# Kernel optimization log

Measured on AMD Instinct MI355X. Metric: run time of the kernel, lower is better.

## Reference

```python
import jax, jax.numpy as jnp
import numpy as np

N_NODES = 100000
N_EDGES = 1600000
IN_DIM = 48
HID = 16
N_CLASSES = 8


def _sage_conv(x, src, dst, W_l, W_r, b, n_nodes):
    # PyG SAGEConv (aggr='mean', root_weight=True):
    #   out_i = W_l @ mean_{j in N(i)} x_j + b + W_r @ x_i
    msg = x[src]                                              # [E, F]
    agg = jax.ops.segment_sum(msg, dst, num_segments=n_nodes)  # [N, F]
    deg = jax.ops.segment_sum(jnp.ones((src.shape[0],), x.dtype), dst,
                              num_segments=n_nodes)            # [N]
    agg = agg / jnp.maximum(deg, 1.0)[:, None]
    return agg @ W_l.T + b + x @ W_r.T


def setup_inputs() -> dict:
    key = jax.random.key(0)
    ks = jax.random.split(key, 10)
    def lin(k, out_d, in_d):
        s = 1.0 / np.sqrt(in_d)
        return jax.random.uniform(k, (out_d, in_d), jnp.float32, -s, s)
    x = jax.random.normal(ks[0], (N_NODES, IN_DIM), jnp.float32)
    edge_index = jax.random.randint(ks[1], (2, N_EDGES), 0, N_NODES, jnp.int64)
    return {
        "x": x,
        "edge_index": edge_index,
        "W1_l": lin(ks[2], HID, IN_DIM), "W1_r": lin(ks[3], HID, IN_DIM),
        "b1": jnp.zeros((HID,), jnp.float32),
        "W2_l": lin(ks[4], HID, HID), "W2_r": lin(ks[5], HID, HID),
        "b2": jnp.zeros((HID,), jnp.float32),
        "W3_l": lin(ks[6], N_CLASSES, HID), "W3_r": lin(ks[7], N_CLASSES, HID),
        "b3": jnp.zeros((N_CLASSES,), jnp.float32),
    }


def reference(x, edge_index, W1_l, W1_r, b1, W2_l, W2_r, b2, W3_l, W3_r, b3):
    src, dst = edge_index[0], edge_index[1]
    n = x.shape[0]
    # dropout is identity in deterministic/eval reference
    h = jax.nn.elu(_sage_conv(x, src, dst, W1_l, W1_r, b1, n))
    h = jax.nn.elu(_sage_conv(h, src, dst, W2_l, W2_r, b2, n))
    h = jax.nn.elu(_sage_conv(h, src, dst, W3_l, W3_r, b3, n))
    return jax.nn.log_softmax(h, axis=-1)
```

## Files before the change

kernel.cpp:

```cpp
#include <hip/hip_runtime.h>
#include <hip/hip_bf16.h>
#include <math.h>

#define N_IN   48
#define N_HID  16
#define N_CLS  8
#define CAP    48
#define NB_SHIFT 9
#define TILE   4096
#define CAPB   9216
#define WSTR   52

__device__ __forceinline__ float bf2f(unsigned short u) {
    union { unsigned int i; float f; } c;
    c.i = ((unsigned int)u) << 16;
    return c.f;
}
__device__ __forceinline__ unsigned short f2bf(float f) {
    unsigned int u = __float_as_uint(f);
    unsigned int r = u + 0x7FFFu + ((u >> 16) & 1u);
    return (unsigned short)(r >> 16);
}

__device__ __forceinline__ void acc16(const ushort4* __restrict__ P4,
        unsigned mul, unsigned q,
        int4 a0, int4 a1, int4 a2, int4 a3, float4& acc) {
    ushort4 t0 = P4[(unsigned)a0.x * mul + q];
    ushort4 t1 = P4[(unsigned)a0.y * mul + q];
    ushort4 t2 = P4[(unsigned)a0.z * mul + q];
    ushort4 t3 = P4[(unsigned)a0.w * mul + q];
    ushort4 t4 = P4[(unsigned)a1.x * mul + q];
    ushort4 t5 = P4[(unsigned)a1.y * mul + q];
    ushort4 t6 = P4[(unsigned)a1.z * mul + q];
    ushort4 t7 = P4[(unsigned)a1.w * mul + q];
    ushort4 t8 = P4[(unsigned)a2.x * mul + q];
    ushort4 t9 = P4[(unsigned)a2.y * mul + q];
    ushort4 ta = P4[(unsigned)a2.z * mul + q];
    ushort4 tb = P4[(unsigned)a2.w * mul + q];
    ushort4 tc = P4[(unsigned)a3.x * mul + q];
    ushort4 td = P4[(unsigned)a3.y * mul + q];
    ushort4 te = P4[(unsigned)a3.z * mul + q];
    ushort4 tf = P4[(unsigned)a3.w * mul + q];
    acc.x += ((((bf2f(t0.x)+bf2f(t1.x))+(bf2f(t2.x)+bf2f(t3.x)))
             + ((bf2f(t4.x)+bf2f(t5.x))+(bf2f(t6.x)+bf2f(t7.x))))
            + (((bf2f(t8.x)+bf2f(t9.x))+(bf2f(ta.x)+bf2f(tb.x)))
             + ((bf2f(tc.x)+bf2f(td.x))+(bf2f(te.x)+bf2f(tf.x)))));
    acc.y += ((((bf2f(t0.y)+bf2f(t1.y))+(bf2f(t2.y)+bf2f(t3.y)))
             + ((bf2f(t4.y)+bf2f(t5.y))+(bf2f(t6.y)+bf2f(t7.y))))
            + (((bf2f(t8.y)+bf2f(t9.y))+(bf2f(ta.y)+bf2f(tb.y)))
             + ((bf2f(tc.y)+bf2f(td.y))+(bf2f(te.y)+bf2f(tf.y)))));
    acc.z += ((((bf2f(t0.z)+bf2f(t1.z))+(bf2f(t2.z)+bf2f(t3.z)))
             + ((bf2f(t4.z)+bf2f(t5.z))+(bf2f(t6.z)+bf2f(t7.z))))
            + (((bf2f(t8.z)+bf2f(t9.z))+(bf2f(ta.z)+bf2f(tb.z)))
             + ((bf2f(tc.z)+bf2f(td.z))+(bf2f(te.z)+bf2f(tf.z)))));
    acc.w += ((((bf2f(t0.w)+bf2f(t1.w))+(bf2f(t2.w)+bf2f(t3.w)))
             + ((bf2f(t4.w)+bf2f(t5.w))+(bf2f(t6.w)+bf2f(t7.w))))
            + (((bf2f(t8.w)+bf2f(t9.w))+(bf2f(ta.w)+bf2f(tb.w)))
             + ((bf2f(tc.w)+bf2f(td.w))+(bf2f(te.w)+bf2f(tf.w)))));
}

__device__ __forceinline__ void acc8(const ushort4* __restrict__ P4,
        unsigned mul, unsigned q,
        int4 a0, int4 a1, float4& acc) {
    ushort4 t0 = P4[(unsigned)a0.x * mul + q];
    ushort4 t1 = P4[(unsigned)a0.y * mul + q];
    ushort4 t2 = P4[(unsigned)a0.z * mul + q];
    ushort4 t3 = P4[(unsigned)a0.w * mul + q];
    ushort4 t4 = P4[(unsigned)a1.x * mul + q];
    ushort4 t5 = P4[(unsigned)a1.y * mul + q];
    ushort4 t6 = P4[(unsigned)a1.z * mul + q];
    ushort4 t7 = P4[(unsigned)a1.w * mul + q];
    acc.x += ((bf2f(t0.x)+bf2f(t1.x))+(bf2f(t2.x)+bf2f(t3.x)))
           + ((bf2f(t4.x)+bf2f(t5.x))+(bf2f(t6.x)+bf2f(t7.x)));
    acc.y += ((bf2f(t0.y)+bf2f(t1.y))+(bf2f(t2.y)+bf2f(t3.y)))
           + ((bf2f(t4.y)+bf2f(t5.y))+(bf2f(t6.y)+bf2f(t7.y)));
    acc.z += ((bf2f(t0.z)+bf2f(t1.z))+(bf2f(t2.z)+bf2f(t3.z)))
           + ((bf2f(t4.z)+bf2f(t5.z))+(bf2f(t6.z)+bf2f(t7.z)));
    acc.w += ((bf2f(t0.w)+bf2f(t1.w))+(bf2f(t2.w)+bf2f(t3.w)))
           + ((bf2f(t4.w)+bf2f(t5.w))+(bf2f(t6.w)+bf2f(t7.w)));
}

__global__ __launch_bounds__(256) void scatter_tiles_kernel(
        const int* __restrict__ src, const int* __restrict__ dst,
        int* __restrict__ cursor, int* __restrict__ ebuf, int E) {
    __shared__ int lh[256];
    __shared__ int gbase[256];
    __shared__ int rank[256];
    int t = threadIdx.x;
    lh[t] = 0;
    rank[t] = 0;
    __syncthreads();
    int base = blockIdx.x * TILE;
    int dcache[TILE / 256];
#pragma unroll
    for (int k = 0; k < TILE / 256; k++) {
        int e = base + t + k * 256;
        dcache[k] = -1;
        if (e < E) {
            int d = dst[e];
            dcache[k] = d;
            atomicAdd(&lh[d >> NB_SHIFT], 1);
        }
    }
    __syncthreads();
    if (lh[t]) gbase[t] = atomicAdd(&cursor[t], lh[t]);
    __syncthreads();
#pragma unroll
    for (int k = 0; k < TILE / 256; k++) {
        int e = base + t + k * 256;
        if (e < E) {
            int d = dcache[k];
            int b = d >> NB_SHIFT;
            int r = gbase[b] + atomicAdd(&rank[b], 1);
            if (r < CAPB)
                ebuf[b * CAPB + r] = ((d & 511) << 17) | src[e];
        }
    }
}

__global__ __launch_bounds__(256) void fill_proj_kernel(
        const int* __restrict__ cursor, const int* __restrict__ ebuf,
        int* __restrict__ cnt, int* __restrict__ adj,
        const float* __restrict__ X,
        const float* __restrict__ Wl, const float* __restrict__ Wr,
        const float* __restrict__ b,
        unsigned short* __restrict__ P, unsigned short* __restrict__ S,
        int N, int nbuck) {
    __shared__ int   lc[512];
    __shared__ float sWl[N_HID * WSTR];
    __shared__ float sWr[N_HID * WSTR];
    __shared__ float sb[N_HID];
    int t = threadIdx.x;

    if ((int)blockIdx.x < nbuck) {
        int bb = blockIdx.x;
        int nodeBeg = bb << NB_SHIFT;
        for (int i = t; i < 512; i += 256) lc[i] = 0;
        __syncthreads();
        int nb = cursor[bb];
        if (nb > CAPB) nb = CAPB;
        int beg = bb * CAPB, end = beg + nb;
        for (int e = beg + t; e < end; e += 256) {
            int v = ebuf[e];
            int ld = ((unsigned int)v) >> 17;
            int s  = v & 0x1FFFF;
            int p = atomicAdd(&lc[ld], 1);
            if (p < CAP) adj[(size_t)(nodeBeg + ld) * CAP + p] = s;
        }
        __syncthreads();
        for (int i = t; i < 512; i += 256) {
            int node = nodeBeg + i;
            if (node >= N) continue;
            int c = lc[i];
            cnt[node] = c;
            if (c > CAP) c = CAP;
            int degp = (c + 15) & ~15;
            if (degp < 16) degp = 16;
            int* row = adj + (size_t)node * CAP;
            for (int p = c; p < degp; p++) row[p] = N;
        }
        return;
    }

    for (int idx = t; idx < N_HID * N_IN; idx += 256) {
        int r = idx / N_IN, k = idx - r * N_IN;
        sWl[r * WSTR + k] = Wl[idx];
        sWr[r * WSTR + k] = Wr[idx];
    }
    if (t < N_HID) sb[t] = b[t];
    __syncthreads();

    int node = ((int)blockIdx.x - nbuck) * 64 + (t >> 2);
    int q = t & 3;
    if (node > N) return;
    int gid = node * 4 + q;
    if (node == N) {
        reinterpret_cast<ushort4*>(P)[gid] = make_ushort4(0, 0, 0, 0);
        reinterpret_cast<ushort4*>(S)[gid] = make_ushort4(0, 0, 0, 0);
        return;
    }

    const float4* xrow = reinterpret_cast<const float4*>(X + (size_t)node * N_IN);
    float accL[4], accR[4];
#pragma unroll
    for (int oo = 0; oo < 4; oo++) { accL[oo] = 0.0f; accR[oo] = sb[4 * q + oo]; }

#pragma unroll
    for (int c = 0; c < N_IN / 4; c++) {
        float4 xv = xrow[c];
#pragma unroll
        for (int oo = 0; oo < 4; oo++) {
            int row = 4 * q + oo;
            float4 wl = *reinterpret_cast<const float4*>(&sWl[row * WSTR + 4 * c]);
            float4 wr = *reinterpret_cast<const float4*>(&sWr[row * WSTR + 4 * c]);
            accL[oo] = fmaf(xv.x, wl.x, accL[oo]); accR[oo] = fmaf(xv.x, wr.x, accR[oo]);
            accL[oo] = fmaf(xv.y, wl.y, accL[oo]); accR[oo] = fmaf(xv.y, wr.y, accR[oo]);
            accL[oo] = fmaf(xv.z, wl.z, accL[oo]); accR[oo] = fmaf(xv.z, wr.z, accR[oo]);
            accL[oo] = fmaf(xv.w, wl.w, accL[oo]); accR[oo] = fmaf(xv.w, wr.w, accR[oo]);
        }
    }

    reinterpret_cast<ushort4*>(P)[gid] =
        make_ushort4(f2bf(accL[0]), f2bf(accL[1]), f2bf(accL[2]), f2bf(accL[3]));
    reinterpret_cast<ushort4*>(S)[gid] =
        make_ushort4(f2bf(accR[0]), f2bf(accR[1]), f2bf(accR[2]), f2bf(accR[3]));
}

__global__ __launch_bounds__(256, 6) void gather_proj16_kernel(
        const int* __restrict__ cnt, const int* __restrict__ adj,
        const unsigned short* __restrict__ Pin, const unsigned short* __restrict__ Sin,
        const float* __restrict__ Wl, const float* __restrict__ Wr,
        const float* __restrict__ bias,
        unsigned short* __restrict__ Pout, unsigned short* __restrict__ Sout, int N) {
    int gid = blockIdx.x * blockDim.x + threadIdx.x;
    if (gid >= N * 4) return;
    if (gid < 4)
        reinterpret_cast<ushort4*>(Pout)[(unsigned)N * 4u + gid] = make_ushort4(0, 0, 0, 0);
    int i = gid >> 2;
    unsigned q = gid & 3;
    int deg = cnt[i];
    if (deg > CAP) deg = CAP;
    int degp = (deg + 15) & ~15;
    if (degp < 16) degp = 16;
    const int4* lst4 = reinterpret_cast<const int4*>(adj) + (unsigned)i * (CAP / 4);
    int4 a0 = lst4[0], a1 = lst4[1], a2 = lst4[2], a3 = lst4[3];
    ushort4 svu = reinterpret_cast<const ushort4*>(Sin)[(unsigned)gid];
    const ushort4* P4 = reinterpret_cast<const ushort4*>(Pin);
    float4 acc = make_float4(0.f, 0.f, 0.f, 0.f);
    int4 b0, b1, b2, b3;
    if (degp > 16) { b0 = lst4[4]; b1 = lst4[5]; b2 = lst4[6]; b3 = lst4[7]; }
    acc16(P4, 4u, q, a0, a1, a2, a3, acc);
    if (degp > 16) {
        acc16(P4, 4u, q, b0, b1, b2, b3, acc);
        if (degp > 32)
            acc16(P4, 4u, q, lst4[8], lst4[9], lst4[10], lst4[11], acc);
    }
    float inv = 1.0f / (float)max(deg, 1);
    float4 h;
    h.x = acc.x * inv + bf2f(svu.x); h.y = acc.y * inv + bf2f(svu.y);
    h.z = acc.z * inv + bf2f(svu.z); h.w = acc.w * inv + bf2f(svu.w);
    h.x = h.x > 0.f ? h.x : expm1f(h.x);
    h.y = h.y > 0.f ? h.y : expm1f(h.y);
    h.z = h.z > 0.f ? h.z : expm1f(h.z);
    h.w = h.w > 0.f ? h.w : expm1f(h.w);

    int lane = threadIdx.x & 63;
    int lb = lane & ~3;
    float hv[16];
#pragma unroll
    for (int a = 0; a < 4; a++) {
        hv[4 * a + 0] = __shfl(h.x, lb + a, 64);
        hv[4 * a + 1] = __shfl(h.y, lb + a, 64);
        hv[4 * a + 2] = __shfl(h.z, lb + a, 64);
        hv[4 * a + 3] = __shfl(h.w, lb + a, 64);
    }

    const float4* Wl4 = reinterpret_cast<const float4*>(Wl);
    const float4* Wr4 = reinterpret_cast<const float4*>(Wr);
    float pl[4], sr[4];
#pragma unroll
    for (int oo = 0; oo < 4; oo++) {
        int o = 4 * q + oo;
        float aL = 0.0f, aR = bias[o];
#pragma unroll
        for (int c = 0; c < 4; c++) {
            float4 wl = Wl4[o * 4 + c];
            float4 wr = Wr4[o * 4 + c];
            aL = fmaf(hv[4 * c + 0], wl.x, aL); aR = fmaf(hv[4 * c + 0], wr.x, aR);
            aL = fmaf(hv[4 * c + 1], wl.y, aL); aR = fmaf(hv[4 * c + 1], wr.y, aR);
            aL = fmaf(hv[4 * c + 2], wl.z, aL); aR = fmaf(hv[4 * c + 2], wr.z, aR);
            aL = fmaf(hv[4 * c + 3], wl.w, aL); aR = fmaf(hv[4 * c + 3], wr.w, aR);
        }
        pl[oo] = aL; sr[oo] = aR;
    }
    reinterpret_cast<ushort4*>(Pout)[(unsigned)gid] =
        make_ushort4(f2bf(pl[0]), f2bf(pl[1]), f2bf(pl[2]), f2bf(pl[3]));
    reinterpret_cast<ushort4*>(Sout)[(unsigned)gid] =
        make_ushort4(f2bf(sr[0]), f2bf(sr[1]), f2bf(sr[2]), f2bf(sr[3]));
}

__global__ __launch_bounds__(256, 6) void gather_proj8_kernel(
        const int* __restrict__ cnt, const int* __restrict__ adj,
        const unsigned short* __restrict__ Pin, const unsigned short* __restrict__ Sin,
        const float* __restrict__ Wl, const float* __restrict__ Wr,
        const float* __restrict__ bias,
        unsigned int* __restrict__ Pout, unsigned int* __restrict__ Sout, int N) {
    int gid = blockIdx.x * blockDim.x + threadIdx.x;
    if (gid >= N * 4) return;
    if (gid < 4)
        Pout[(unsigned)N * 4u + gid] = 0u;
    int i = gid >> 2;
    unsigned q = gid & 3;
    int deg = cnt[i];
    if (deg > CAP) deg = CAP;
    int degp = (deg + 15) & ~15;
    if (degp < 16) degp = 16;
    const int4* lst4 = reinterpret_cast<const int4*>(adj) + (unsigned)i * (CAP / 4);
    int4 a0 = lst4[0], a1 = lst4[1], a2 = lst4[2], a3 = lst4[3];
    ushort4 svu = reinterpret_cast<const ushort4*>(Sin)[(unsigned)gid];
    const ushort4* P4 = reinterpret_cast<const ushort4*>(Pin);
    float4 acc = make_float4(0.f, 0.f, 0.f, 0.f);
    int4 b0, b1, b2, b3;
    if (degp > 16) { b0 = lst4[4]; b1 = lst4[5]; b2 = lst4[6]; b3 = lst4[7]; }
    acc16(P4, 4u, q, a0, a1, a2, a3, acc);
    if (degp > 16) {
        acc16(P4, 4u, q, b0, b1, b2, b3, acc);
        if (degp > 32)
            acc16(P4, 4u, q, lst4[8], lst4[9], lst4[10], lst4[11], acc);
    }
    float inv = 1.0f / (float)max(deg, 1);
    float4 h;
    h.x = acc.x * inv + bf2f(svu.x); h.y = acc.y * inv + bf2f(svu.y);
    h.z = acc.z * inv + bf2f(svu.z); h.w = acc.w * inv + bf2f(svu.w);
    h.x = h.x > 0.f ? h.x : expm1f(h.x);
    h.y = h.y > 0.f ? h.y : expm1f(h.y);
    h.z = h.z > 0.f ? h.z : expm1f(h.z);
    h.w = h.w > 0.f ? h.w : expm1f(h.w);

    int lane = threadIdx.x & 63;
    int lb = lane & ~3;
    float hv[16];
#pragma unroll
    for (int a = 0; a < 4; a++) {
        hv[4 * a + 0] = __shfl(h.x, lb + a, 64);
        hv[4 * a + 1] = __shfl(h.y, lb + a, 64);
        hv[4 * a + 2] = __shfl(h.z, lb + a, 64);
        hv[4 * a + 3] = __shfl(h.w, lb + a, 64);
    }

    const float4* Wl4 = reinterpret_cast<const float4*>(Wl);
    const float4* Wr4 = reinterpret_cast<const float4*>(Wr);
    float pl[2], sr[2];
#pragma unroll
    for (int oo = 0; oo < 2; oo++) {
        int o = 2 * q + oo;
        float aL = 0.0f, aR = bias[o];
#pragma unroll
        for (int c = 0; c < 4; c++) {
            float4 wl = Wl4[o * 4 + c];
            float4 wr = Wr4[o * 4 + c];
            aL = fmaf(hv[4 * c + 0], wl.x, aL); aR = fmaf(hv[4 * c + 0], wr.x, aR);
            aL = fmaf(hv[4 * c + 1], wl.y, aL); aR = fmaf(hv[4 * c + 1], wr.y, aR);
            aL = fmaf(hv[4 * c + 2], wl.z, aL); aR = fmaf(hv[4 * c + 2], wr.z, aR);
            aL = fmaf(hv[4 * c + 3], wl.w, aL); aR = fmaf(hv[4 * c + 3], wr.w, aR);
        }
        pl[oo] = aL; sr[oo] = aR;
    }
    Pout[(unsigned)gid] = ((unsigned int)f2bf(pl[1]) << 16) | f2bf(pl[0]);
    Sout[(unsigned)gid] = ((unsigned int)f2bf(sr[1]) << 16) | f2bf(sr[0]);
}

__global__ __launch_bounds__(256, 6) void gather8_kernel(
        const int* __restrict__ cnt, const int* __restrict__ adj,
        const unsigned short* __restrict__ P, const unsigned short* __restrict__ S,
        float* __restrict__ out, int N) {
    int t = blockIdx.x * blockDim.x + threadIdx.x;
    if (t >= N * 4) return;
    int i = t >> 2;
    unsigned sub = t & 3;
    unsigned q  = sub & 1;
    unsigned hf = sub >> 1;
    int deg = cnt[i];
    if (deg > CAP) deg = CAP;
    int degp = (deg + 15) & ~15;
    if (degp < 16) degp = 16;
    const int4* lst4 = reinterpret_cast<const int4*>(adj) + (unsigned)i * (CAP / 4);
    ushort4 svu = reinterpret_cast<const ushort4*>(S)[(unsigned)i * 2u + q];
    const ushort4* P4 = reinterpret_cast<const ushort4*>(P);
    float4 acc = make_float4(0.f, 0.f, 0.f, 0.f);
    if (degp == 16) {
        acc8(P4, 2u, q, lst4[hf * 2 + 0], lst4[hf * 2 + 1], acc);
    } else {
        acc16(P4, 2u, q, lst4[hf * 4 + 0], lst4[hf * 4 + 1],
                          lst4[hf * 4 + 2], lst4[hf * 4 + 3], acc);
        if (degp > 32)
            acc8(P4, 2u, q, lst4[8 + hf * 2], lst4[9 + hf * 2], acc);
    }
    acc.x += __shfl_xor(acc.x, 2, 64);
    acc.y += __shfl_xor(acc.y, 2, 64);
    acc.z += __shfl_xor(acc.z, 2, 64);
    acc.w += __shfl_xor(acc.w, 2, 64);

    float inv = 1.0f / (float)max(deg, 1);
    float4 v;
    v.x = acc.x * inv + bf2f(svu.x); v.y = acc.y * inv + bf2f(svu.y);
    v.z = acc.z * inv + bf2f(svu.z); v.w = acc.w * inv + bf2f(svu.w);
    v.x = v.x > 0.f ? v.x : expm1f(v.x);
    v.y = v.y > 0.f ? v.y : expm1f(v.y);
    v.z = v.z > 0.f ? v.z : expm1f(v.z);
    v.w = v.w > 0.f ? v.w : expm1f(v.w);
    float m = fmaxf(fmaxf(v.x, v.y), fmaxf(v.z, v.w));
    m = fmaxf(m, __shfl_xor(m, 1, 64));
    float sum = expf(v.x - m) + expf(v.y - m) + expf(v.z - m) + expf(v.w - m);
    sum += __shfl_xor(sum, 1, 64);
    float lse = m + logf(sum);
    if (hf == 0)
        reinterpret_cast<float4*>(out)[(unsigned)i * 2u + q] =
            make_float4(v.x - lse, v.y - lse, v.z - lse, v.w - lse);
}

extern "C" void kernel_launch(void* const* d_in, const int* in_sizes, int n_in,
                              void* d_out, int out_size, void* d_ws, size_t ws_size,
                              hipStream_t stream) {
    const float* x   = (const float*)d_in[0];
    const int*   ei  = (const int*)d_in[1];
    const float* W1l = (const float*)d_in[2];
    const float* W1r = (const float*)d_in[3];
    const float* b1  = (const float*)d_in[4];
    const float* W2l = (const float*)d_in[5];
    const float* W2r = (const float*)d_in[6];
    const float* b2  = (const float*)d_in[7];
    const float* W3l = (const float*)d_in[8];
    const float* W3r = (const float*)d_in[9];
    const float* b3  = (const float*)d_in[10];
    float* out = (float*)d_out;

    const int N = in_sizes[0] / N_IN;
    const int E = in_sizes[1] / 2;
    const int* src = ei;
    const int* dst = ei + E;
    const int nbuck = (N + 511) >> NB_SHIFT;

    int* cursor = (int*)d_ws;
    int* cnt    = cursor + 256;
    int  Npad   = (N + 3) & ~3;
    int* adj    = cnt + Npad;
    int* ebuf   = adj + (size_t)N * CAP;
    const size_t Nr = (size_t)N + 1;
    unsigned short* P1 = (unsigned short*)(ebuf + (size_t)nbuck * CAPB);
    unsigned short* P2 = P1 + Nr * N_HID;
    unsigned short* S1 = P2 + Nr * N_HID;
    unsigned short* S3 = S1 + Nr * N_HID;
    unsigned short* P3 = P1;

    hipMemsetAsync(cursor, 0, 256 * sizeof(int), stream);

    const int B = 256;
    int n4Grid   = (N * 4 + B - 1) / B;
    int p1Grid   = (N + 1 + 63) / 64;
    int tileGrid = (E + TILE - 1) / TILE;

    scatter_tiles_kernel<<<tileGrid, B, 0, stream>>>(src, dst, cursor, ebuf, E);

    fill_proj_kernel<<<nbuck + p1Grid, B, 0, stream>>>(
        cursor, ebuf, cnt, adj, x, W1l, W1r, b1, P1, S1, N, nbuck);

    gather_proj16_kernel<<<n4Grid, B, 0, stream>>>(cnt, adj, P1, S1,
                                                   W2l, W2r, b2, P2, S1, N);

    gather_proj8_kernel<<<n4Grid, B, 0, stream>>>(cnt, adj, P2, S1,
                                                  W3l, W3r, b3,
                                                  (unsigned int*)P3,
                                                  (unsigned int*)S3, N);

    gather8_kernel<<<n4Grid, B, 0, stream>>>(cnt, adj, P3, S3, out, N);
}
```

Measured before the change: 212.3 us.

## Replace two-pass bucketed adjacency build with direct global-atomic scatter

Drops the tiled bucket-scatter kernel and its intermediate edge buffer. Each edge now does a global atomicAdd on its destination's counter and writes straight into the fixed-capacity adjacency row. Padding is done in a separate per-node pass merged with the layer-1 projection. This removes one pass over the edges and the staging buffer, but trades LDS atomics for 1.6M contended global atomics with scattered writes, and needs a larger memset of the counters.

Result: slower. 308.5 us (+45.3%).

```diff
diff --git a/kernel.cpp b/kernel.cpp
--- a/kernel.cpp
+++ b/kernel.cpp
@@ -6,9 +6,6 @@
 #define N_HID  16
 #define N_CLS  8
 #define CAP    48
-#define NB_SHIFT 9
-#define TILE   4096
-#define CAPB   9216
 #define WSTR   52
 
 __device__ __forceinline__ float bf2f(unsigned short u) {
@@ -80,85 +77,38 @@
            + ((bf2f(t4.w)+bf2f(t5.w))+(bf2f(t6.w)+bf2f(t7.w)));
 }
 
-__global__ __launch_bounds__(256) void scatter_tiles_kernel(
+__global__ __launch_bounds__(256) void build_adj_kernel(
         const int* __restrict__ src, const int* __restrict__ dst,
-        int* __restrict__ cursor, int* __restrict__ ebuf, int E) {
-    __shared__ int lh[256];
-    __shared__ int gbase[256];
-    __shared__ int rank[256];
-    int t = threadIdx.x;
-    lh[t] = 0;
-    rank[t] = 0;
-    __syncthreads();
-    int base = blockIdx.x * TILE;
-    int dcache[TILE / 256];
-#pragma unroll
-    for (int k = 0; k < TILE / 256; k++) {
-        int e = base + t + k * 256;
-        dcache[k] = -1;
-        if (e < E) {
-            int d = dst[e];
-            dcache[k] = d;
-            atomicAdd(&lh[d >> NB_SHIFT], 1);
-        }
-    }
-    __syncthreads();
-    if (lh[t]) gbase[t] = atomicAdd(&cursor[t], lh[t]);
-    __syncthreads();
-#pragma unroll
-    for (int k = 0; k < TILE / 256; k++) {
-        int e = base + t + k * 256;
-        if (e < E) {
-            int d = dcache[k];
-            int b = d >> NB_SHIFT;
-            int r = gbase[b] + atomicAdd(&rank[b], 1);
-            if (r < CAPB)
-                ebuf[b * CAPB + r] = ((d & 511) << 17) | src[e];
-        }
-    }
-}
-
-__global__ __launch_bounds__(256) void fill_proj_kernel(
-        const int* __restrict__ cursor, const int* __restrict__ ebuf,
-        int* __restrict__ cnt, int* __restrict__ adj,
+        int* __restrict__ cnt, int* __restrict__ adj, int E) {
+    int e = blockIdx.x * 256 + threadIdx.x;
+    if (e >= E) return;
+    int d = dst[e];
+    int s = src[e];
+    int p = atomicAdd(&cnt[d], 1);
+    if (p < CAP) adj[(unsigned)d * CAP + p] = s;
+}
+
+__global__ __launch_bounds__(256) void pad_proj_kernel(
+        const int* __restrict__ cnt, int* __restrict__ adj,
         const float* __restrict__ X,
         const float* __restrict__ Wl, const float* __restrict__ Wr,
         const float* __restrict__ b,
         unsigned short* __restrict__ P, unsigned short* __restrict__ S,
-        int N, int nbuck) {
-    __shared__ int   lc[512];
+        int N, int padGrid) {
     __shared__ float sWl[N_HID * WSTR];
     __shared__ float sWr[N_HID * WSTR];
     __shared__ float sb[N_HID];
     int t = threadIdx.x;
 
-    if ((int)blockIdx.x < nbuck) {
-        int bb = blockIdx.x;
-        int nodeBeg = bb << NB_SHIFT;
-        for (int i = t; i < 512; i += 256) lc[i] = 0;
-        __syncthreads();
-        int nb = cursor[bb];
-        if (nb > CAPB) nb = CAPB;
-        int beg = bb * CAPB, end = beg + nb;
-        for (int e = beg + t; e < end; e += 256) {
-            int v = ebuf[e];
-            int ld = ((unsigned int)v) >> 17;
-            int s  = v & 0x1FFFF;
-            int p = atomicAdd(&lc[ld], 1);
-            if (p < CAP) adj[(size_t)(nodeBeg + ld) * CAP + p] = s;
-        }
-        __syncthreads();
-        for (int i = t; i < 512; i += 256) {
-            int node = nodeBeg + i;
-            if (node >= N) continue;
-            int c = lc[i];
-            cnt[node] = c;
-            if (c > CAP) c = CAP;
-            int degp = (c + 15) & ~15;
-            if (degp < 16) degp = 16;
-            int* row = adj + (size_t)node * CAP;
-            for (int p = c; p < degp; p++) row[p] = N;
-        }
+    if ((int)blockIdx.x < padGrid) {
+        int i = blockIdx.x * 256 + t;
+        if (i >= N) return;
+        int c = cnt[i];
+        if (c > CAP) c = CAP;
+        int degp = (c + 15) & ~15;
+        if (degp < 16) degp = 16;
+        int* row = adj + (unsigned)i * CAP;
+        for (int p = c; p < degp; p++) row[p] = N;
         return;
     }
 
@@ -170,7 +120,7 @@
     if (t < N_HID) sb[t] = b[t];
     __syncthreads();
 
-    int node = ((int)blockIdx.x - nbuck) * 64 + (t >> 2);
+    int node = ((int)blockIdx.x - padGrid) * 64 + (t >> 2);
     int q = t & 3;
     if (node > N) return;
     int gid = node * 4 + q;
@@ -419,31 +369,29 @@
     const int E = in_sizes[1] / 2;
     const int* src = ei;
     const int* dst = ei + E;
-    const int nbuck = (N + 511) >> NB_SHIFT;
-
-    int* cursor = (int*)d_ws;
-    int* cnt    = cursor + 256;
+
+    int* cnt    = (int*)d_ws;
     int  Npad   = (N + 3) & ~3;
     int* adj    = cnt + Npad;
-    int* ebuf   = adj + (size_t)N * CAP;
     const size_t Nr = (size_t)N + 1;
-    unsigned short* P1 = (unsigned short*)(ebuf + (size_t)nbuck * CAPB);
+    unsigned short* P1 = (unsigned short*)(adj + (size_t)N * CAP);
     unsigned short* P2 = P1 + Nr * N_HID;
     unsigned short* S1 = P2 + Nr * N_HID;
     unsigned short* S3 = S1 + Nr * N_HID;
     unsigned short* P3 = P1;
 
-    hipMemsetAsync(cursor, 0, 256 * sizeof(int), stream);
+    hipMemsetAsync(cnt, 0, (size_t)Npad * sizeof(int), stream);
 
     const int B = 256;
     int n4Grid   = (N * 4 + B - 1) / B;
     int p1Grid   = (N + 1 + 63) / 64;
-    int tileGrid = (E + TILE - 1) / TILE;
-
-    scatter_tiles_kernel<<<tileGrid, B, 0, stream>>>(src, dst, cursor, ebuf, E);
-
-    fill_proj_kernel<<<nbuck + p1Grid, B, 0, stream>>>(
-        cursor, ebuf, cnt, adj, x, W1l, W1r, b1, P1, S1, N, nbuck);
+    int padGrid  = (N + B - 1) / B;
+    int eGrid    = (E + B - 1) / B;
+
+    build_adj_kernel<<<eGrid, B, 0, stream>>>(src, dst, cnt, adj, E);
+
+    pad_proj_kernel<<<padGrid + p1Grid, B, 0, stream>>>(
+        cnt, adj, x, W1l, W1r, b1, P1, S1, N, padGrid);
 
     gather_proj16_kernel<<<n4Grid, B, 0, stream>>>(cnt, adj, P1, S1,
                                                    W2l, W2r, b2, P2, S1, N);
```

## Fuse all GNN stages into one cooperative persistent kernel with grid syncs

Applied to the files above, without the earlier changes.

Turns the scatter, fill/projection, and three gather stages into device functions and runs them inside a single cooperative persistent kernel of 1024 blocks, separated by grid-wide syncs, with the original multi-kernel path kept as a fallback if the cooperative launch fails. It also overlaps the edge scatter with the first-layer projection in the same phase. The aim is to remove per-kernel launch gaps and tail drain between the five stages. In exchange, grid syncs add their own cost, occupancy is capped by launch_bounds(256,4) and the combined shared-memory footprint, and grid-stride loops may spread work less evenly than separate launches.

New measurement: 747.3 us. 252% more time.

```diff
diff --git a/kernel.cpp b/kernel.cpp
--- a/kernel.cpp
+++ b/kernel.cpp
@@ -1,6 +1,9 @@
 #include <hip/hip_runtime.h>
+#include <hip/hip_cooperative_groups.h>
 #include <hip/hip_bf16.h>
 #include <math.h>
+
+namespace cg = cooperative_groups;
 
 #define N_IN   48
 #define N_HID  16
@@ -80,17 +83,13 @@
            + ((bf2f(t4.w)+bf2f(t5.w))+(bf2f(t6.w)+bf2f(t7.w)));
 }
 
-__global__ __launch_bounds__(256) void scatter_tiles_kernel(
+__device__ __forceinline__ void scatter_tile_body(int tileId, int t,
         const int* __restrict__ src, const int* __restrict__ dst,
-        int* __restrict__ cursor, int* __restrict__ ebuf, int E) {
-    __shared__ int lh[256];
-    __shared__ int gbase[256];
-    __shared__ int rank[256];
-    int t = threadIdx.x;
-    lh[t] = 0;
-    rank[t] = 0;
-    __syncthreads();
-    int base = blockIdx.x * TILE;
+        int* __restrict__ cursor, int* __restrict__ ebuf, int E,
+        int* lh, int* gbase, int* rank) {
+    lh[t] = 0; rank[t] = 0;
+    __syncthreads();
+    int base = tileId * TILE;
     int dcache[TILE / 256];
 #pragma unroll
     for (int k = 0; k < TILE / 256; k++) {
@@ -116,75 +115,54 @@
                 ebuf[b * CAPB + r] = ((d & 511) << 17) | src[e];
         }
     }
-}
-
-__global__ __launch_bounds__(256) void fill_proj_kernel(
+    __syncthreads();
+}
+
+__device__ __forceinline__ void fill_bucket_body(int bb, int t,
         const int* __restrict__ cursor, const int* __restrict__ ebuf,
-        int* __restrict__ cnt, int* __restrict__ adj,
-        const float* __restrict__ X,
-        const float* __restrict__ Wl, const float* __restrict__ Wr,
-        const float* __restrict__ b,
-        unsigned short* __restrict__ P, unsigned short* __restrict__ S,
-        int N, int nbuck) {
-    __shared__ int   lc[512];
-    __shared__ float sWl[N_HID * WSTR];
-    __shared__ float sWr[N_HID * WSTR];
-    __shared__ float sb[N_HID];
-    int t = threadIdx.x;
-
-    if ((int)blockIdx.x < nbuck) {
-        int bb = blockIdx.x;
-        int nodeBeg = bb << NB_SHIFT;
-        for (int i = t; i < 512; i += 256) lc[i] = 0;
-        __syncthreads();
-        int nb = cursor[bb];
-        if (nb > CAPB) nb = CAPB;
-        int beg = bb * CAPB, end = beg + nb;
-        for (int e = beg + t; e < end; e += 256) {
-            int v = ebuf[e];
-            int ld = ((unsigned int)v) >> 17;
-            int s  = v & 0x1FFFF;
-            int p = atomicAdd(&lc[ld], 1);
-            if (p < CAP) adj[(size_t)(nodeBeg + ld) * CAP + p] = s;
-        }
-        __syncthreads();
-        for (int i = t; i < 512; i += 256) {
-            int node = nodeBeg + i;
-            if (node >= N) continue;
-            int c = lc[i];
-            cnt[node] = c;
-            if (c > CAP) c = CAP;
-            int degp = (c + 15) & ~15;
-            if (degp < 16) degp = 16;
-            int* row = adj + (size_t)node * CAP;
-            for (int p = c; p < degp; p++) row[p] = N;
-        }
-        return;
-    }
-
-    for (int idx = t; idx < N_HID * N_IN; idx += 256) {
-        int r = idx / N_IN, k = idx - r * N_IN;
-        sWl[r * WSTR + k] = Wl[idx];
-        sWr[r * WSTR + k] = Wr[idx];
-    }
-    if (t < N_HID) sb[t] = b[t];
-    __syncthreads();
-
-    int node = ((int)blockIdx.x - nbuck) * 64 + (t >> 2);
-    int q = t & 3;
-    if (node > N) return;
+        int* __restrict__ cnt, int* __restrict__ adj, int N, int* lc) {
+    int nodeBeg = bb << NB_SHIFT;
+    for (int i = t; i < 512; i += 256) lc[i] = 0;
+    __syncthreads();
+    int nb = cursor[bb];
+    if (nb > CAPB) nb = CAPB;
+    int beg = bb * CAPB, end = beg + nb;
+    for (int e = beg + t; e < end; e += 256) {
+        int v = ebuf[e];
+        int ld = ((unsigned int)v) >> 17;
+        int s  = v & 0x1FFFF;
+        int p = atomicAdd(&lc[ld], 1);
+        if (p < CAP) adj[(size_t)(nodeBeg + ld) * CAP + p] = s;
+    }
+    __syncthreads();
+    for (int i = t; i < 512; i += 256) {
+        int node = nodeBeg + i;
+        if (node >= N) continue;
+        int c = lc[i];
+        cnt[node] = c;
+        if (c > CAP) c = CAP;
+        int degp = (c + 15) & ~15;
+        if (degp < 16) degp = 16;
+        int* row = adj + (size_t)node * CAP;
+        for (int p = c; p < degp; p++) row[p] = N;
+    }
+    __syncthreads();
+}
+
+__device__ __forceinline__ void proj48_body(int node, int q,
+        const float* __restrict__ X, const float* sWl, const float* sWr,
+        const float* sb, unsigned short* __restrict__ P,
+        unsigned short* __restrict__ S, int N) {
     int gid = node * 4 + q;
     if (node == N) {
         reinterpret_cast<ushort4*>(P)[gid] = make_ushort4(0, 0, 0, 0);
         reinterpret_cast<ushort4*>(S)[gid] = make_ushort4(0, 0, 0, 0);
         return;
     }
-
     const float4* xrow = reinterpret_cast<const float4*>(X + (size_t)node * N_IN);
     float accL[4], accR[4];
 #pragma unroll
     for (int oo = 0; oo < 4; oo++) { accL[oo] = 0.0f; accR[oo] = sb[4 * q + oo]; }
-
 #pragma unroll
     for (int c = 0; c < N_IN / 4; c++) {
         float4 xv = xrow[c];
@@ -199,23 +177,18 @@
             accL[oo] = fmaf(xv.w, wl.w, accL[oo]); accR[oo] = fmaf(xv.w, wr.w, accR[oo]);
         }
     }
-
     reinterpret_cast<ushort4*>(P)[gid] =
         make_ushort4(f2bf(accL[0]), f2bf(accL[1]), f2bf(accL[2]), f2bf(accL[3]));
     reinterpret_cast<ushort4*>(S)[gid] =
         make_ushort4(f2bf(accR[0]), f2bf(accR[1]), f2bf(accR[2]), f2bf(accR[3]));
 }
 
-__global__ __launch_bounds__(256, 6) void gather_proj16_kernel(
+__device__ __forceinline__ void gp16_body(int gid, int t,
         const int* __restrict__ cnt, const int* __restrict__ adj,
         const unsigned short* __restrict__ Pin, const unsigned short* __restrict__ Sin,
         const float* __restrict__ Wl, const float* __restrict__ Wr,
         const float* __restrict__ bias,
         unsigned short* __restrict__ Pout, unsigned short* __restrict__ Sout, int N) {
-    int gid = blockIdx.x * blockDim.x + threadIdx.x;
-    if (gid >= N * 4) return;
-    if (gid < 4)
-        reinterpret_cast<ushort4*>(Pout)[(unsigned)N * 4u + gid] = make_ushort4(0, 0, 0, 0);
     int i = gid >> 2;
     unsigned q = gid & 3;
     int deg = cnt[i];
@@ -244,7 +217,7 @@
     h.z = h.z > 0.f ? h.z : expm1f(h.z);
     h.w = h.w > 0.f ? h.w : expm1f(h.w);
 
-    int lane = threadIdx.x & 63;
+    int lane = t & 63;
     int lb = lane & ~3;
     float hv[16];
 #pragma unroll
@@ -279,16 +252,12 @@
         make_ushort4(f2bf(sr[0]), f2bf(sr[1]), f2bf(sr[2]), f2bf(sr[3]));
 }
 
-__global__ __launch_bounds__(256, 6) void gather_proj8_kernel(
+__device__ __forceinline__ void gp8_body(int gid, int t,
         const int* __restrict__ cnt, const int* __restrict__ adj,
         const unsigned short* __restrict__ Pin, const unsigned short* __restrict__ Sin,
         const float* __restrict__ Wl, const float* __restrict__ Wr,
         const float* __restrict__ bias,
         unsigned int* __restrict__ Pout, unsigned int* __restrict__ Sout, int N) {
-    int gid = blockIdx.x * blockDim.x + threadIdx.x;
-    if (gid >= N * 4) return;
-    if (gid < 4)
-        Pout[(unsigned)N * 4u + gid] = 0u;
     int i = gid >> 2;
     unsigned q = gid & 3;
     int deg = cnt[i];
@@ -317,7 +286,7 @@
     h.z = h.z > 0.f ? h.z : expm1f(h.z);
     h.w = h.w > 0.f ? h.w : expm1f(h.w);
 
-    int lane = threadIdx.x & 63;
+    int lane = t & 63;
     int lb = lane & ~3;
     float hv[16];
 #pragma unroll
@@ -350,14 +319,12 @@
     Sout[(unsigned)gid] = ((unsigned int)f2bf(sr[1]) << 16) | f2bf(sr[0]);
 }
 
-__global__ __launch_bounds__(256, 6) void gather8_kernel(
+__device__ __forceinline__ void g8_body(int tg, int t,
         const int* __restrict__ cnt, const int* __restrict__ adj,
         const unsigned short* __restrict__ P, const unsigned short* __restrict__ S,
         float* __restrict__ out, int N) {
-    int t = blockIdx.x * blockDim.x + threadIdx.x;
-    if (t >= N * 4) return;
-    int i = t >> 2;
-    unsigned sub = t & 3;
+    int i = tg >> 2;
+    unsigned sub = tg & 3;
     unsigned q  = sub & 1;
     unsigned hf = sub >> 1;
     int deg = cnt[i];
@@ -399,6 +366,158 @@
             make_float4(v.x - lse, v.y - lse, v.z - lse, v.w - lse);
 }
 
+struct MegaParams {
+    const float* x; const int* src; const int* dst;
+    const float *W1l, *W1r, *b1, *W2l, *W2r, *b2, *W3l, *W3r, *b3;
+    float* out;
+    int* cursor; int* cnt; int* adj; int* ebuf;
+    unsigned short *P1, *P2, *S1, *S3;
+    int N, E, nTiles, nbuck, projUnits, n4Units;
+};
+
+__global__ __launch_bounds__(256, 4) void mega_kernel(MegaParams p) {
+    cg::grid_group grid = cg::this_grid();
+    const int t = threadIdx.x;
+    const int G = gridDim.x;
+
+    __shared__ int lh[256], gbase[256], rank[256];
+    __shared__ int lc[512];
+    __shared__ float sWl[N_HID * WSTR];
+    __shared__ float sWr[N_HID * WSTR];
+    __shared__ float sb[N_HID];
+
+    for (int idx = t; idx < N_HID * N_IN; idx += 256) {
+        int r = idx / N_IN, k = idx - r * N_IN;
+        sWl[r * WSTR + k] = p.W1l[idx];
+        sWr[r * WSTR + k] = p.W1r[idx];
+    }
+    if (t < N_HID) sb[t] = p.b1[t];
+    __syncthreads();
+
+    int U1 = p.nTiles + p.projUnits;
+    for (int u = blockIdx.x; u < U1; u += G) {
+        if (u < p.nTiles) {
+            scatter_tile_body(u, t, p.src, p.dst, p.cursor, p.ebuf, p.E,
+                              lh, gbase, rank);
+        } else {
+            int pu = u - p.nTiles;
+            int node = pu * 64 + (t >> 2);
+            int q = t & 3;
+            if (node <= p.N)
+                proj48_body(node, q, p.x, sWl, sWr, sb, p.P1, p.S1, p.N);
+        }
+    }
+    grid.sync();
+
+    for (int bb = blockIdx.x; bb < p.nbuck; bb += G)
+        fill_bucket_body(bb, t, p.cursor, p.ebuf, p.cnt, p.adj, p.N, lc);
+    grid.sync();
+
+    for (int u = blockIdx.x; u < p.n4Units; u += G) {
+        int gid = u * 256 + t;
+        if (gid < 4)
+            reinterpret_cast<ushort4*>(p.P2)[(unsigned)p.N * 4u + gid] =
+                make_ushort4(0, 0, 0, 0);
+        if (gid < p.N * 4)
+            gp16_body(gid, t, p.cnt, p.adj, p.P1, p.S1,
+                      p.W2l, p.W2r, p.b2, p.P2, p.S1, p.N);
+    }
+    grid.sync();
+
+    unsigned int* P3out = (unsigned int*)p.P1;
+    unsigned int* S3out = (unsigned int*)p.S3;
+    for (int u = blockIdx.x; u < p.n4Units; u += G) {
+        int gid = u * 256 + t;
+        if (gid < 4)
+            P3out[(unsigned)p.N * 4u + gid] = 0u;
+        if (gid < p.N * 4)
+            gp8_body(gid, t, p.cnt, p.adj, p.P2, p.S1,
+                     p.W3l, p.W3r, p.b3, P3out, S3out, p.N);
+    }
+    grid.sync();
+
+    const unsigned short* P3 = p.P1;
+    const unsigned short* S3 = (const unsigned short*)p.S3;
+    for (int u = blockIdx.x; u < p.n4Units; u += G) {
+        int tg = u * 256 + t;
+        if (tg < p.N * 4)
+            g8_body(tg, t, p.cnt, p.adj, P3, S3, p.out, p.N);
+    }
+}
+
+__global__ __launch_bounds__(256) void scatter_tiles_kernel(
+        const int* __restrict__ src, const int* __restrict__ dst,
+        int* __restrict__ cursor, int* __restrict__ ebuf, int E) {
+    __shared__ int lh[256], gbase[256], rank[256];
+    scatter_tile_body(blockIdx.x, threadIdx.x, src, dst, cursor, ebuf, E,
+                      lh, gbase, rank);
+}
+
+__global__ __launch_bounds__(256) void fill_proj_kernel(
+        const int* __restrict__ cursor, const int* __restrict__ ebuf,
+        int* __restrict__ cnt, int* __restrict__ adj,
+        const float* __restrict__ X,
+        const float* __restrict__ Wl, const float* __restrict__ Wr,
+        const float* __restrict__ b,
+        unsigned short* __restrict__ P, unsigned short* __restrict__ S,
+        int N, int nbuck) {
+    __shared__ int lc[512];
+    __shared__ float sWl[N_HID * WSTR];
+    __shared__ float sWr[N_HID * WSTR];
+    __shared__ float sb[N_HID];
+    int t = threadIdx.x;
+    if ((int)blockIdx.x < nbuck) {
+        fill_bucket_body(blockIdx.x, t, cursor, ebuf, cnt, adj, N, lc);
+        return;
+    }
+    for (int idx = t; idx < N_HID * N_IN; idx += 256) {
+        int r = idx / N_IN, k = idx - r * N_IN;
+        sWl[r * WSTR + k] = Wl[idx];
+        sWr[r * WSTR + k] = Wr[idx];
+    }
+    if (t < N_HID) sb[t] = b[t];
+    __syncthreads();
+    int node = ((int)blockIdx.x - nbuck) * 64 + (t >> 2);
+    int q = t & 3;
+    if (node <= N)
+        proj48_body(node, q, X, sWl, sWr, sb, P, S, N);
+}
+
+__global__ __launch_bounds__(256, 6) void gather_proj16_kernel(
+        const int* __restrict__ cnt, const int* __restrict__ adj,
+        const unsigned short* __restrict__ Pin, const unsigned short* __restrict__ Sin,
+        const float* __restrict__ Wl, const float* __restrict__ Wr,
+        const float* __restrict__ bias,
+        unsigned short* __restrict__ Pout, unsigned short* __restrict__ Sout, int N) {
+    int gid = blockIdx.x * blockDim.x + threadIdx.x;
+    if (gid >= N * 4) return;
+    if (gid < 4)
+        reinterpret_cast<ushort4*>(Pout)[(unsigned)N * 4u + gid] = make_ushort4(0, 0, 0, 0);
+    gp16_body(gid, threadIdx.x, cnt, adj, Pin, Sin, Wl, Wr, bias, Pout, Sout, N);
+}
+
+__global__ __launch_bounds__(256, 6) void gather_proj8_kernel(
+        const int* __restrict__ cnt, const int* __restrict__ adj,
+        const unsigned short* __restrict__ Pin, const unsigned short* __restrict__ Sin,
+        const float* __restrict__ Wl, const float* __restrict__ Wr,
+        const float* __restrict__ bias,
+        unsigned int* __restrict__ Pout, unsigned int* __restrict__ Sout, int N) {
+    int gid = blockIdx.x * blockDim.x + threadIdx.x;
+    if (gid >= N * 4) return;
+    if (gid < 4)
+        Pout[(unsigned)N * 4u + gid] = 0u;
+    gp8_body(gid, threadIdx.x, cnt, adj, Pin, Sin, Wl, Wr, bias, Pout, Sout, N);
+}
+
+__global__ __launch_bounds__(256, 6) void gather8_kernel(
+        const int* __restrict__ cnt, const int* __restrict__ adj,
+        const unsigned short* __restrict__ P, const unsigned short* __restrict__ S,
+        float* __restrict__ out, int N) {
+    int tg = blockIdx.x * blockDim.x + threadIdx.x;
+    if (tg >= N * 4) return;
+    g8_body(tg, threadIdx.x, cnt, adj, P, S, out, N);
+}
+
 extern "C" void kernel_launch(void* const* d_in, const int* in_sizes, int n_in,
                               void* d_out, int out_size, void* d_ws, size_t ws_size,
                               hipStream_t stream) {
@@ -431,7 +550,6 @@
     unsigned short* P2 = P1 + Nr * N_HID;
     unsigned short* S1 = P2 + Nr * N_HID;
     unsigned short* S3 = S1 + Nr * N_HID;
-    unsigned short* P3 = P1;
 
     hipMemsetAsync(cursor, 0, 256 * sizeof(int), stream);
 
@@ -440,18 +558,31 @@
     int p1Grid   = (N + 1 + 63) / 64;
     int tileGrid = (E + TILE - 1) / TILE;
 
-    scatter_tiles_kernel<<<tileGrid, B, 0, stream>>>(src, dst, cursor, ebuf, E);
-
-    fill_proj_kernel<<<nbuck + p1Grid, B, 0, stream>>>(
-        cursor, ebuf, cnt, adj, x, W1l, W1r, b1, P1, S1, N, nbuck);
-
-    gather_proj16_kernel<<<n4Grid, B, 0, stream>>>(cnt, adj, P1, S1,
-                                                   W2l, W2r, b2, P2, S1, N);
-
-    gather_proj8_kernel<<<n4Grid, B, 0, stream>>>(cnt, adj, P2, S1,
-                                                  W3l, W3r, b3,
-                                                  (unsigned int*)P3,
-                                                  (unsigned int*)S3, N);
-
-    gather8_kernel<<<n4Grid, B, 0, stream>>>(cnt, adj, P3, S3, out, N);
-}
+    MegaParams mp;
+    mp.x = x; mp.src = src; mp.dst = dst;
+    mp.W1l = W1l; mp.W1r = W1r; mp.b1 = b1;
+    mp.W2l = W2l; mp.W2r = W2r; mp.b2 = b2;
+    mp.W3l = W3l; mp.W3r = W3r; mp.b3 = b3;
+    mp.out = out;
+    mp.cursor = cursor; mp.cnt = cnt; mp.adj = adj; mp.ebuf = ebuf;
+    mp.P1 = P1; mp.P2 = P2; mp.S1 = S1; mp.S3 = S3;
+    mp.N = N; mp.E = E; mp.nTiles = tileGrid; mp.nbuck = nbuck;
+    mp.projUnits = p1Grid; mp.n4Units = n4Grid;
+
+    void* args[] = { &mp };
+    hipError_t err = hipLaunchCooperativeKernel(
+        (const void*)mega_kernel, dim3(1024), dim3(256), args, 0, stream);
+
+    if (err != hipSuccess) {
+        scatter_tiles_kernel<<<tileGrid, B, 0, stream>>>(src, dst, cursor, ebuf, E);
+        fill_proj_kernel<<<nbuck + p1Grid, B, 0, stream>>>(
+            cursor, ebuf, cnt, adj, x, W1l, W1r, b1, P1, S1, N, nbuck);
+        gather_proj16_kernel<<<n4Grid, B, 0, stream>>>(cnt, adj, P1, S1,
+                                                       W2l, W2r, b2, P2, S1, N);
+        gather_proj8_kernel<<<n4Grid, B, 0, stream>>>(cnt, adj, P2, S1,
+                                                      W3l, W3r, b3,
+                                                      (unsigned int*)P1,
+                                                      (unsigned int*)S3, N);
+        gather8_kernel<<<n4Grid, B, 0, stream>>>(cnt, adj, P1, S3, out, N);
+    }
+}
```

## Fuse layer-1 projection into scatter kernel and halve bucket size for fill

Applied to the files above, without the earlier changes.

Moves the layer-1 dense projection blocks out of the fill kernel and into the edge-scatter kernel's grid, so the projection runs concurrently with the bucketing pass. The fill stage becomes its own kernel. Buckets now cover 256 nodes instead of 512, giving about twice as many fill blocks (~391 vs ~196) for better occupancy on the device. The cost is a larger cursor histogram and more global atomics per tile in the scatter kernel. The per-bucket capacity also shrinks to 4800 edges, which leaves less headroom for overflow on skewed degree distributions.

Result: no change. 211.3 us (-0.4%).

```diff
diff --git a/kernel.cpp b/kernel.cpp
--- a/kernel.cpp
+++ b/kernel.cpp
@@ -6,9 +6,10 @@
 #define N_HID  16
 #define N_CLS  8
 #define CAP    48
-#define NB_SHIFT 9
+#define NB_SHIFT 8
+#define NBH    512
 #define TILE   4096
-#define CAPB   9216
+#define CAPB   4800
 #define WSTR   52
 
 __device__ __forceinline__ float bf2f(unsigned short u) {
@@ -80,84 +81,51 @@
            + ((bf2f(t4.w)+bf2f(t5.w))+(bf2f(t6.w)+bf2f(t7.w)));
 }
 
-__global__ __launch_bounds__(256) void scatter_tiles_kernel(
+__global__ __launch_bounds__(256) void scatter_proj_kernel(
         const int* __restrict__ src, const int* __restrict__ dst,
-        int* __restrict__ cursor, int* __restrict__ ebuf, int E) {
-    __shared__ int lh[256];
-    __shared__ int gbase[256];
-    __shared__ int rank[256];
-    int t = threadIdx.x;
-    lh[t] = 0;
-    rank[t] = 0;
-    __syncthreads();
-    int base = blockIdx.x * TILE;
-    int dcache[TILE / 256];
-#pragma unroll
-    for (int k = 0; k < TILE / 256; k++) {
-        int e = base + t + k * 256;
-        dcache[k] = -1;
-        if (e < E) {
-            int d = dst[e];
-            dcache[k] = d;
-            atomicAdd(&lh[d >> NB_SHIFT], 1);
-        }
-    }
-    __syncthreads();
-    if (lh[t]) gbase[t] = atomicAdd(&cursor[t], lh[t]);
-    __syncthreads();
-#pragma unroll
-    for (int k = 0; k < TILE / 256; k++) {
-        int e = base + t + k * 256;
-        if (e < E) {
-            int d = dcache[k];
-            int b = d >> NB_SHIFT;
-            int r = gbase[b] + atomicAdd(&rank[b], 1);
-            if (r < CAPB)
-                ebuf[b * CAPB + r] = ((d & 511) << 17) | src[e];
-        }
-    }
-}
-
-__global__ __launch_bounds__(256) void fill_proj_kernel(
-        const int* __restrict__ cursor, const int* __restrict__ ebuf,
-        int* __restrict__ cnt, int* __restrict__ adj,
+        int* __restrict__ cursor, int* __restrict__ ebuf, int E,
         const float* __restrict__ X,
         const float* __restrict__ Wl, const float* __restrict__ Wr,
         const float* __restrict__ b,
         unsigned short* __restrict__ P, unsigned short* __restrict__ S,
-        int N, int nbuck) {
-    __shared__ int   lc[512];
+        int N, int nTiles) {
+    __shared__ int lh[NBH];
+    __shared__ int gbase[NBH];
+    __shared__ int rank_[NBH];
     __shared__ float sWl[N_HID * WSTR];
     __shared__ float sWr[N_HID * WSTR];
     __shared__ float sb[N_HID];
     int t = threadIdx.x;
 
-    if ((int)blockIdx.x < nbuck) {
-        int bb = blockIdx.x;
-        int nodeBeg = bb << NB_SHIFT;
-        for (int i = t; i < 512; i += 256) lc[i] = 0;
+    if ((int)blockIdx.x < nTiles) {
+        for (int i = t; i < NBH; i += 256) { lh[i] = 0; rank_[i] = 0; }
         __syncthreads();
-        int nb = cursor[bb];
-        if (nb > CAPB) nb = CAPB;
-        int beg = bb * CAPB, end = beg + nb;
-        for (int e = beg + t; e < end; e += 256) {
-            int v = ebuf[e];
-            int ld = ((unsigned int)v) >> 17;
-            int s  = v & 0x1FFFF;
-            int p = atomicAdd(&lc[ld], 1);
-            if (p < CAP) adj[(size_t)(nodeBeg + ld) * CAP + p] = s;
+        int base = blockIdx.x * TILE;
+        int dcache[TILE / 256];
+#pragma unroll
+        for (int k = 0; k < TILE / 256; k++) {
+            int e = base + t + k * 256;
+            dcache[k] = -1;
+            if (e < E) {
+                int d = dst[e];
+                dcache[k] = d;
+                atomicAdd(&lh[d >> NB_SHIFT], 1);
+            }
         }
         __syncthreads();
-        for (int i = t; i < 512; i += 256) {
-            int node = nodeBeg + i;
-            if (node >= N) continue;
-            int c = lc[i];
-            cnt[node] = c;
-            if (c > CAP) c = CAP;
-            int degp = (c + 15) & ~15;
-            if (degp < 16) degp = 16;
-            int* row = adj + (size_t)node * CAP;
-            for (int p = c; p < degp; p++) row[p] = N;
+        for (int i = t; i < NBH; i += 256)
+            if (lh[i]) gbase[i] = atomicAdd(&cursor[i], lh[i]);
+        __syncthreads();
+#pragma unroll
+        for (int k = 0; k < TILE / 256; k++) {
+            int e = base + t + k * 256;
+            if (e < E) {
+                int d = dcache[k];
+                int bk = d >> NB_SHIFT;
+                int r = gbase[bk] + atomicAdd(&rank_[bk], 1);
+                if (r < CAPB)
+                    ebuf[bk * CAPB + r] = ((d & 255) << 17) | src[e];
+            }
         }
         return;
     }
@@ -170,7 +138,7 @@
     if (t < N_HID) sb[t] = b[t];
     __syncthreads();
 
-    int node = ((int)blockIdx.x - nbuck) * 64 + (t >> 2);
+    int node = ((int)blockIdx.x - nTiles) * 64 + (t >> 2);
     int q = t & 3;
     if (node > N) return;
     int gid = node * 4 + q;
@@ -204,6 +172,38 @@
         make_ushort4(f2bf(accL[0]), f2bf(accL[1]), f2bf(accL[2]), f2bf(accL[3]));
     reinterpret_cast<ushort4*>(S)[gid] =
         make_ushort4(f2bf(accR[0]), f2bf(accR[1]), f2bf(accR[2]), f2bf(accR[3]));
+}
+
+__global__ __launch_bounds__(256) void fill_pad_kernel(
+        const int* __restrict__ cursor, const int* __restrict__ ebuf,
+        int* __restrict__ cnt, int* __restrict__ adj, int N) {
+    __shared__ int lc[256];
+    int t = threadIdx.x;
+    int bb = blockIdx.x;
+    int nodeBeg = bb << NB_SHIFT;
+    lc[t] = 0;
+    __syncthreads();
+    int nb = cursor[bb];
+    if (nb > CAPB) nb = CAPB;
+    int beg = bb * CAPB, end = beg + nb;
+    for (int e = beg + t; e < end; e += 256) {
+        int v = ebuf[e];
+        int ld = ((unsigned int)v) >> 17;
+        int s  = v & 0x1FFFF;
+        int p = atomicAdd(&lc[ld], 1);
+        if (p < CAP) adj[(size_t)(nodeBeg + ld) * CAP + p] = s;
+    }
+    __syncthreads();
+    int node = nodeBeg + t;
+    if (node < N) {
+        int c = lc[t];
+        cnt[node] = c;
+        if (c > CAP) c = CAP;
+        int degp = (c + 15) & ~15;
+        if (degp < 16) degp = 16;
+        int* row = adj + (size_t)node * CAP;
+        for (int p = c; p < degp; p++) row[p] = N;
+    }
 }
 
 __global__ __launch_bounds__(256, 6) void gather_proj16_kernel(
@@ -419,10 +419,10 @@
     const int E = in_sizes[1] / 2;
     const int* src = ei;
     const int* dst = ei + E;
-    const int nbuck = (N + 511) >> NB_SHIFT;
+    const int nbuck = (N + 255) >> NB_SHIFT;
 
     int* cursor = (int*)d_ws;
-    int* cnt    = cursor + 256;
+    int* cnt    = cursor + NBH;
     int  Npad   = (N + 3) & ~3;
     int* adj    = cnt + Npad;
     int* ebuf   = adj + (size_t)N * CAP;
@@ -433,17 +433,17 @@
     unsigned short* S3 = S1 + Nr * N_HID;
     unsigned short* P3 = P1;
 
-    hipMemsetAsync(cursor, 0, 256 * sizeof(int), stream);
+    hipMemsetAsync(cursor, 0, NBH * sizeof(int), stream);
 
     const int B = 256;
     int n4Grid   = (N * 4 + B - 1) / B;
     int p1Grid   = (N + 1 + 63) / 64;
     int tileGrid = (E + TILE - 1) / TILE;
 
-    scatter_tiles_kernel<<<tileGrid, B, 0, stream>>>(src, dst, cursor, ebuf, E);
-
-    fill_proj_kernel<<<nbuck + p1Grid, B, 0, stream>>>(
-        cursor, ebuf, cnt, adj, x, W1l, W1r, b1, P1, S1, N, nbuck);
+    scatter_proj_kernel<<<tileGrid + p1Grid, B, 0, stream>>>(
+        src, dst, cursor, ebuf, E, x, W1l, W1r, b1, P1, S1, N, tileGrid);
+
+    fill_pad_kernel<<<nbuck, B, 0, stream>>>(cursor, ebuf, cnt, adj, N);
 
     gather_proj16_kernel<<<n4Grid, B, 0, stream>>>(cnt, adj, P1, S1,
                                                    W2l, W2r, b2, P2, S1, N);
```
